# Kernel optimization log

Hardware: AMD Instinct MI355X
Metric: run time of the kernel (lower is better)

## Reference

```python
import jax, jax.numpy as jnp
import numpy as np

N = 100000   # nodes
E = 3200000  # edges
R = 8        # relations
F_IN = 128
DIMS = 64
C = 40


def setup_inputs() -> dict:
    key = jax.random.key(0)
    ks = jax.random.split(key, 10)
    s = 0.1
    return {
        "x": jax.random.normal(ks[0], (N, F_IN), jnp.float32),
        "edge_index": jax.random.randint(ks[1], (2, E), 0, N),
        "edge_weight": jax.random.uniform(ks[2], (E,), jnp.float32),
        "edge_color": jax.random.randint(ks[3], (E,), 0, R),
        "W1_rel": jax.random.normal(ks[4], (R, F_IN, DIMS), jnp.float32) * s,
        "W1_root": jax.random.normal(ks[5], (F_IN, DIMS), jnp.float32) * s,
        "b1": jnp.zeros((DIMS,), jnp.float32),
        "W2_rel": jax.random.normal(ks[6], (R, DIMS, C), jnp.float32) * s,
        "W2_root": jax.random.normal(ks[7], (DIMS, C), jnp.float32) * s,
        "b2": jnp.zeros((C,), jnp.float32),
    }


def _wrgcn_layer(x, src, dst, edge_weight, edge_color, W_rel, W_root, b):
    # Transform all nodes under every relation weight: [R, N, O]
    h = jnp.einsum('nf,rfo->rno', x, W_rel)
    # Gather per-edge message using (relation, source) indexing, weight it: [E, O]
    msg = h[edge_color, src] * edge_weight[:, None]
    # Scatter-add weighted messages to destination nodes
    agg = jnp.zeros((x.shape[0], W_rel.shape[2]), x.dtype).at[dst].add(msg)
    # Root (self) transform + bias
    return agg + x @ W_root + b


def reference(x, edge_index, edge_weight, edge_color, W1_rel, W1_root, b1, W2_rel, W2_root, b2):
    src, dst = edge_index[0], edge_index[1]
    h = jax.nn.relu(_wrgcn_layer(x, src, dst, edge_weight, edge_color, W1_rel, W1_root, b1))
    # dropout p=0 (eval): identity
    out = _wrgcn_layer(h, src, dst, edge_weight, edge_color, W2_rel, W2_root, b2)
    return (jax.nn.log_softmax(out, axis=1), out)
```

## Files before the change

kernel.cpp:

```cpp
#include <hip/hip_runtime.h>
#include <hip/hip_bf16.h>
#include <cmath>


#define RELS 8
#define CH 4096
#define ST2CAP 6144

typedef __attribute__((ext_vector_type(8))) short bf16x8;
typedef __attribute__((ext_vector_type(4))) float f32x4;

static __device__ __forceinline__ ushort f2bf(float f) {
    __hip_bfloat16 b = __float2bfloat16(f);
    return *reinterpret_cast<ushort*>(&b);
}
static __device__ __forceinline__ float bf2f(ushort u) {
    return __uint_as_float(((unsigned int)u) << 16);
}

__global__ __launch_bounds__(256) void cast_f32_bf16x4(
    const float* __restrict__ in, ushort* __restrict__ out, int n4)
{
    int i = blockIdx.x * 256 + threadIdx.x;
    if (i >= n4) return;
    float4 v = ((const float4*)in)[i];
    ushort4 o;
    o.x = f2bf(v.x); o.y = f2bf(v.y); o.z = f2bf(v.z); o.w = f2bf(v.w);
    ((ushort4*)out)[i] = o;
}

__global__ __launch_bounds__(256) void cast_relu_bf16x4(
    const float* __restrict__ in, ushort* __restrict__ out, int n4)
{
    int i = blockIdx.x * 256 + threadIdx.x;
    if (i >= n4) return;
    float4 v = ((const float4*)in)[i];
    ushort4 o;
    o.x = f2bf(fmaxf(v.x, 0.f)); o.y = f2bf(fmaxf(v.y, 0.f));
    o.z = f2bf(fmaxf(v.z, 0.f)); o.w = f2bf(fmaxf(v.w, 0.f));
    ((ushort4*)out)[i] = o;
}

__global__ __launch_bounds__(256) void conv_w1(
    const float* __restrict__ Wrel, const float* __restrict__ Wroot,
    ushort* __restrict__ wt)
{
    int i = blockIdx.x * 256 + threadIdx.x;
    if (i >= 9 * 64 * 128) return;
    int r = i >> 13, c = (i >> 7) & 63, k = i & 127;
    float v = (r < 8) ? Wrel[((size_t)r * 128 + k) * 64 + c]
                      : Wroot[(size_t)k * 64 + c];
    wt[i] = f2bf(v);
}

__global__ __launch_bounds__(256) void conv_w2(
    const float* __restrict__ Wrel, const float* __restrict__ Wroot,
    ushort* __restrict__ wt)
{
    int i = blockIdx.x * 256 + threadIdx.x;
    if (i >= 9 * 48 * 64) return;
    int r = i / (48 * 64), rem = i - r * (48 * 64);
    int c = rem >> 6, k = rem & 63;
    float v = 0.f;
    if (c < 40)
        v = (r < 8) ? Wrel[((size_t)r * 64 + k) * 40 + c]
                    : Wroot[(size_t)k * 40 + c];
    wt[i] = f2bf(v);
}

__global__ __launch_bounds__(256) void gemm1_mfma(
    const ushort* __restrict__ xb, const ushort* __restrict__ w1t,
    ushort* __restrict__ hout, float* __restrict__ agg1,
    const float* __restrict__ b1, int nN)
{
    __shared__ ushort xs[64 * 128];
    __shared__ ushort wt[64 * 128];
    const int y    = blockIdx.y;
    const int tid  = threadIdx.x;
    const int n0   = blockIdx.x * 64;
    const int nmax = nN - n0;
    const bool isroot = (y == 8);
    ushort* out = hout + (size_t)y * nN * 64;
    const ushort* wsrc = w1t + (size_t)y * 64 * 128;

    for (int i = tid; i < 1024; i += 256) {
        int row = i >> 4, ch = i & 15;
        uint4 v = make_uint4(0u, 0u, 0u, 0u);
        if (row < nmax)
            v = *(const uint4*)(xb + (size_t)(n0 + row) * 128 + ch * 8);
        int off = (row * 256 + ch * 16) ^ ((row & 7) << 4);
        *(uint4*)((char*)xs + off) = v;
    }
    for (int i = tid; i < 1024; i += 256) {
        int row = i >> 4, ch = i & 15;
        uint4 v = *(const uint4*)(wsrc + (size_t)row * 128 + ch * 8);
        int off = (row * 256 + ch * 16) ^ ((row & 7) << 4);
        *(uint4*)((char*)wt + off) = v;
    }
    __syncthreads();

    const int wv   = tid >> 6;
    const int lane = tid & 63;
    const int lr   = wv * 16 + (lane & 15);
    const int kgb  = (lane >> 4) * 8;

    f32x4 acc[4] = {{0.f,0.f,0.f,0.f},{0.f,0.f,0.f,0.f},
                    {0.f,0.f,0.f,0.f},{0.f,0.f,0.f,0.f}};

    #pragma unroll
    for (int ks = 0; ks < 4; ++ks) {
        int kb = (ks * 32 + kgb) * 2;
        int aoff = (lr * 256 + kb) ^ ((lr & 7) << 4);
        bf16x8 a = *(const bf16x8*)((const char*)xs + aoff);
        #pragma unroll
        for (int ct = 0; ct < 4; ++ct) {
            int col = ct * 16 + (lane & 15);
            int boff = (col * 256 + kb) ^ ((col & 7) << 4);
            bf16x8 b = *(const bf16x8*)((const char*)wt + boff);
            acc[ct] = __builtin_amdgcn_mfma_f32_16x16x32_bf16(a, b, acc[ct], 0, 0, 0);
        }
    }

    #pragma unroll
    for (int ct = 0; ct < 4; ++ct) {
        int col = ct * 16 + (lane & 15);
        #pragma unroll
        for (int reg = 0; reg < 4; ++reg) {
            int row = wv * 16 + (lane >> 4) * 4 + reg;
            if (row < nmax) {
                if (isroot)
                    agg1[(size_t)(n0 + row) * 64 + col] = acc[ct][reg] + b1[col];
                else
                    out[(size_t)(n0 + row) * 64 + col] = f2bf(acc[ct][reg]);
            }
        }
    }
}

__global__ __launch_bounds__(256) void gemm2_mfma(
    const ushort* __restrict__ y1b, const ushort* __restrict__ w2t,
    ushort* __restrict__ hout, float* __restrict__ agg2,
    const float* __restrict__ b2, int nN)
{
    __shared__ ushort ys[64 * 64];
    __shared__ ushort wt[48 * 64];
    const int y    = blockIdx.y;
    const int tid  = threadIdx.x;
    const int n0   = blockIdx.x * 64;
    const int nmax = nN - n0;
    const bool isroot = (y == 8);
    ushort* out = hout + (size_t)y * nN * 40;
    const ushort* wsrc = w2t + (size_t)y * 48 * 64;

    for (int i = tid; i < 512; i += 256) {
        int row = i >> 3, ch = i & 7;
        uint4 v = make_uint4(0u, 0u, 0u, 0u);
        if (row < nmax)
            v = *(const uint4*)(y1b + (size_t)(n0 + row) * 64 + ch * 8);
        int off = (row * 128 + ch * 16) ^ ((row & 7) << 4);
        *(uint4*)((char*)ys + off) = v;
    }
    for (int i = tid; i < 384; i += 256) {
        int row = i >> 3, ch = i & 7;
        uint4 v = *(const uint4*)(wsrc + (size_t)row * 64 + ch * 8);
        int off = (row * 128 + ch * 16) ^ ((row & 7) << 4);
        *(uint4*)((char*)wt + off) = v;
    }
    __syncthreads();

    const int wv   = tid >> 6;
    const int lane = tid & 63;
    const int lr   = wv * 16 + (lane & 15);
    const int kgb  = (lane >> 4) * 8;

    f32x4 acc[3] = {{0.f,0.f,0.f,0.f},{0.f,0.f,0.f,0.f},{0.f,0.f,0.f,0.f}};

    #pragma unroll
    for (int ks = 0; ks < 2; ++ks) {
        int kb = (ks * 32 + kgb) * 2;
        int aoff = (lr * 128 + kb) ^ ((lr & 7) << 4);
        bf16x8 a = *(const bf16x8*)((const char*)ys + aoff);
        #pragma unroll
        for (int ct = 0; ct < 3; ++ct) {
            int col = ct * 16 + (lane & 15);
            int boff = (col * 128 + kb) ^ ((col & 7) << 4);
            bf16x8 b = *(const bf16x8*)((const char*)wt + boff);
            acc[ct] = __builtin_amdgcn_mfma_f32_16x16x32_bf16(a, b, acc[ct], 0, 0, 0);
        }
    }

    #pragma unroll
    for (int ct = 0; ct < 3; ++ct) {
        int col = ct * 16 + (lane & 15);
        if (col < 40) {
            #pragma unroll
            for (int reg = 0; reg < 4; ++reg) {
                int row = wv * 16 + (lane >> 4) * 4 + reg;
                if (row < nmax) {
                    if (isroot)
                        agg2[(size_t)(n0 + row) * 40 + col] = acc[ct][reg] + b2[col];
                    else
                        out[(size_t)(n0 + row) * 40 + col] = f2bf(acc[ct][reg]);
                }
            }
        }
    }
}

__global__ __launch_bounds__(256) void mcount(
    const int* __restrict__ dst, int* __restrict__ cnt, int nE, int nBkt)
{
    __shared__ int hist[512];
    const int blk = blockIdx.x;
    const int t = threadIdx.x;
    for (int i = t; i < nBkt; i += 256) hist[i] = 0;
    __syncthreads();
    const int e0 = blk * CH;
    const int eend = min(e0 + CH, nE);
    for (int e = e0 + t; e < eend; e += 256)
        atomicAdd(&hist[dst[e] >> 8], 1);
    __syncthreads();
    for (int i = t; i < nBkt; i += 256)
        cnt[(size_t)blk * nBkt + i] = hist[i];
}

__global__ __launch_bounds__(1024) void scanB(
    const int* __restrict__ cnt, int* __restrict__ offm_rel,
    int* __restrict__ tsum, int nBlk, int nBkt)
{
    __shared__ int s[1024];
    const int bkt = blockIdx.x;
    const int t = threadIdx.x;
    int v = (t < nBlk) ? cnt[(size_t)t * nBkt + bkt] : 0;
    s[t] = v; __syncthreads();
    for (int o = 1; o < 1024; o <<= 1) {
        int u = (t >= o) ? s[t - o] : 0;
        __syncthreads(); s[t] += u; __syncthreads();
    }
    if (t < nBlk) offm_rel[(size_t)bkt * nBlk + t] = s[t] - v;
    if (t == nBlk - 1) tsum[bkt] = s[t];
}

__global__ __launch_bounds__(512) void scanT(
    const int* __restrict__ tsum, int* __restrict__ bktbase,
    int* __restrict__ row_off, int nBkt, int nN)
{
    __shared__ int s[512];
    const int t = threadIdx.x;
    int v = (t < nBkt) ? tsum[t] : 0;
    s[t] = v; __syncthreads();
    for (int o = 1; o < 512; o <<= 1) {
        int u = (t >= o) ? s[t - o] : 0;
        __syncthreads(); s[t] += u; __syncthreads();
    }
    if (t < nBkt) bktbase[t] = s[t] - v;
    if (t == nBkt - 1) { bktbase[nBkt] = s[t]; row_off[nN] = s[t]; }
}

__global__ __launch_bounds__(512) void mscatter(
    const int* __restrict__ src, const int* __restrict__ dst,
    const float* __restrict__ ew, const int* __restrict__ ec,
    const int* __restrict__ cnt, const int* __restrict__ offm_rel,
    const int* __restrict__ bktbase,
    uint2* __restrict__ epackA, int nE, int nBlk, int nBkt)
{
    __shared__ uint2 stag[CH];
    __shared__ int lbase[512];
    __shared__ int lcur[512];
    __shared__ int goff[512];
    const int blk = blockIdx.x;
    const int t = threadIdx.x;

    int v = (t < nBkt) ? cnt[(size_t)blk * nBkt + t] : 0;
    lbase[t] = v; __syncthreads();
    for (int o = 1; o < 512; o <<= 1) {
        int u = (t >= o) ? lbase[t - o] : 0;
        __syncthreads(); lbase[t] += u; __syncthreads();
    }
    int excl = lbase[t] - v;
    __syncthreads();
    lbase[t] = excl;
    lcur[t] = excl;
    goff[t] = (t < nBkt) ? bktbase[t] + offm_rel[(size_t)t * nBlk + blk] : 0;
    __syncthreads();

    const int e0 = blk * CH;
    const int eend = min(e0 + CH, nE);
    const int ntot = eend - e0;
    for (int e = e0 + t; e < eend; e += 512) {
        int d = dst[e];
        int bkt = d >> 8;
        unsigned int pk = (unsigned int)src[e] | ((unsigned int)ec[e] << 20)
                        | ((unsigned int)(d & 255) << 23);
        int r = atomicAdd(&lcur[bkt], 1);
        stag[r] = make_uint2(pk, __float_as_uint(ew[e]));
    }
    __syncthreads();
    for (int s2 = t; s2 < ntot; s2 += 512) {
        int lo = 0, hi = nBkt - 1;
        while (lo < hi) {
            int mid = (lo + hi + 1) >> 1;
            if (lbase[mid] <= s2) lo = mid; else hi = mid - 1;
        }
        epackA[goff[lo] + (s2 - lbase[lo])] = stag[s2];
    }
}

__global__ __launch_bounds__(256) void reorder2(
    const uint2* __restrict__ epackA, const int* __restrict__ bktbase,
    int* __restrict__ row_off, uint2* __restrict__ epack, int nN)
{
    __shared__ uint2 stag[ST2CAP];
    __shared__ int hist[256];
    __shared__ int s[256];
    __shared__ int lcur[128];
    const int b    = blockIdx.x;
    const int n0   = b << 7;
    const int pb   = b >> 1;
    const int half = b & 1;
    const int p0 = bktbase[pb];
    const int p1 = bktbase[pb + 1];
    const int t = threadIdx.x;

    hist[t] = 0;
    __syncthreads();
    const unsigned int* ax = (const unsigned int*)epackA;
    for (int e = p0 + t; e < p1; e += 256)
        atomicAdd(&hist[(ax[2 * (size_t)e] >> 23) & 255], 1);
    __syncthreads();
    int v = hist[t];
    s[t] = v; __syncthreads();
    for (int o = 1; o < 256; o <<= 1) {
        int u = (t >= o) ? s[t - o] : 0;
        __syncthreads(); s[t] += u; __syncthreads();
    }
    hist[t] = s[t] - v;
    __syncthreads();

    const int hb0 = hist[half << 7];
    const int hb1 = (half == 0) ? hist[128] : (p1 - p0);
    const int ne  = hb1 - hb0;
    const int s0  = p0 + hb0;

    if (t < 128) {
        int idx = n0 + t;
        if (idx < nN) row_off[idx] = p0 + hist[(half << 7) + t];
        lcur[t] = hist[(half << 7) + t] - hb0;
    }
    __syncthreads();

    if (ne <= ST2CAP) {
        for (int e = p0 + t; e < p1; e += 256) {
            uint2 pw = epackA[e];
            int dl = (pw.x >> 23) & 255;
            if ((dl >> 7) == half) {
                int r = atomicAdd(&lcur[dl & 127], 1);
                stag[r] = pw;
            }
        }
        __syncthreads();
        for (int s2 = t; s2 < ne; s2 += 256)
            epack[s0 + s2] = stag[s2];
    } else {
        if (t < 128) {
            int my = (half << 7) | t;
            int wpos = p0 + hist[my];
            for (int e = p0; e < p1; ++e) {
                uint2 pw = epackA[e];
                if ((int)((pw.x >> 23) & 255) == my) epack[wpos++] = pw;
            }
        }
    }
}

__global__ __launch_bounds__(256) void hist_dst(
    const int* __restrict__ dst, int* __restrict__ counts, int nE)
{
    int e = blockIdx.x * 256 + threadIdx.x;
    if (e < nE) atomicAdd(&counts[dst[e]], 1);
}

__global__ __launch_bounds__(256) void scan_partial(
    const int* __restrict__ counts, int* __restrict__ bsum, int nN)
{
    __shared__ int s[256];
    int t = threadIdx.x;
    int i = blockIdx.x * 256 + t;
    int v = (i < nN) ? counts[i] : 0;
    s[t] = v; __syncthreads();
    for (int o = 1; o < 256; o <<= 1) {
        int u = (t >= o) ? s[t - o] : 0;
        __syncthreads(); s[t] += u; __syncthreads();
    }
    if (t == 255) bsum[blockIdx.x] = s[255];
}

__global__ __launch_bounds__(512) void scan_base(
    const int* __restrict__ bsum, int* __restrict__ bbase, int nb,
    int* __restrict__ row_off, int nN)
{
    __shared__ int s[512];
    int t = threadIdx.x;
    int v = (t < nb) ? bsum[t] : 0;
    s[t] = v; __syncthreads();
    for (int o = 1; o < 512; o <<= 1) {
        int u = (t >= o) ? s[t - o] : 0;
        __syncthreads(); s[t] += u; __syncthreads();
    }
    if (t < nb) bbase[t] = s[t] - v;
    if (t == nb - 1) row_off[nN] = s[t];
}

__global__ __launch_bounds__(256) void scan_final(
    const int* __restrict__ counts, const int* __restrict__ bbase,
    int* __restrict__ row_off, int* __restrict__ cursor, int nN)
{
    __shared__ int s[256];
    int t = threadIdx.x;
    int i = blockIdx.x * 256 + t;
    int v = (i < nN) ? counts[i] : 0;
    s[t] = v; __syncthreads();
    for (int o = 1; o < 256; o <<= 1) {
        int u = (t >= o) ? s[t - o] : 0;
        __syncthreads(); s[t] += u; __syncthreads();
    }
    if (i < nN) {
        int off = bbase[blockIdx.x] + s[t] - v;
        row_off[i] = off;
        cursor[i]  = off;
    }
}

__global__ __launch_bounds__(256) void fill_csr(
    const int* __restrict__ src, const int* __restrict__ dst,
    const float* __restrict__ ew, const int* __restrict__ ec,
    int* __restrict__ cursor, uint2* __restrict__ epack, int nE)
{
    int e = blockIdx.x * 256 + threadIdx.x;
    if (e >= nE) return;
    int p = atomicAdd(&cursor[dst[e]], 1);
    epack[p] = make_uint2((unsigned int)src[e] | ((unsigned int)ec[e] << 20),
                          __float_as_uint(ew[e]));
}

__global__ __launch_bounds__(256) void gather_d64(
    const ushort* __restrict__ h, const int* __restrict__ row_off,
    const uint2* __restrict__ epack, float* __restrict__ agg, int nN)
{
    int w    = (blockIdx.x * 256 + threadIdx.x) >> 6;
    int lane = threadIdx.x & 63;
    if (w >= nN) return;
    int s0 = row_off[w], s1 = row_off[w + 1];
    float acc = agg[(size_t)w * 64 + lane];
    const unsigned int un = (unsigned int)nN;
    for (int base = s0; base < s1; base += 64) {
        int m = min(64, s1 - base);
        unsigned int pk = 0; float wv = 0.f;
        if (lane < m) {
            uint2 pw = epack[base + lane];
            pk = pw.x; wv = __uint_as_float(pw.y);
        }
        int j = 0;
        for (; j + 8 <= m; j += 8) {
            unsigned int p0 = __shfl(pk, j + 0, 64), p1 = __shfl(pk, j + 1, 64);
            unsigned int p2 = __shfl(pk, j + 2, 64), p3 = __shfl(pk, j + 3, 64);
            unsigned int p4 = __shfl(pk, j + 4, 64), p5 = __shfl(pk, j + 5, 64);
            unsigned int p6 = __shfl(pk, j + 6, 64), p7 = __shfl(pk, j + 7, 64);
            float q0 = __shfl(wv, j + 0, 64), q1 = __shfl(wv, j + 1, 64);
            float q2 = __shfl(wv, j + 2, 64), q3 = __shfl(wv, j + 3, 64);
            float q4 = __shfl(wv, j + 4, 64), q5 = __shfl(wv, j + 5, 64);
            float q6 = __shfl(wv, j + 6, 64), q7 = __shfl(wv, j + 7, 64);
            ushort v0 = h[(((p0 >> 20) & 7) * un + (p0 & 0xFFFFFu)) * 64u + lane];
            ushort v1 = h[(((p1 >> 20) & 7) * un + (p1 & 0xFFFFFu)) * 64u + lane];
            ushort v2 = h[(((p2 >> 20) & 7) * un + (p2 & 0xFFFFFu)) * 64u + lane];
            ushort v3 = h[(((p3 >> 20) & 7) * un + (p3 & 0xFFFFFu)) * 64u + lane];
            ushort v4 = h[(((p4 >> 20) & 7) * un + (p4 & 0xFFFFFu)) * 64u + lane];
            ushort v5 = h[(((p5 >> 20) & 7) * un + (p5 & 0xFFFFFu)) * 64u + lane];
            ushort v6 = h[(((p6 >> 20) & 7) * un + (p6 & 0xFFFFFu)) * 64u + lane];
            ushort v7 = h[(((p7 >> 20) & 7) * un + (p7 & 0xFFFFFu)) * 64u + lane];
            acc = fmaf(q0, bf2f(v0), acc); acc = fmaf(q1, bf2f(v1), acc);
            acc = fmaf(q2, bf2f(v2), acc); acc = fmaf(q3, bf2f(v3), acc);
            acc = fmaf(q4, bf2f(v4), acc); acc = fmaf(q5, bf2f(v5), acc);
            acc = fmaf(q6, bf2f(v6), acc); acc = fmaf(q7, bf2f(v7), acc);
        }
        for (; j < m; ++j) {
            unsigned int pj = __shfl(pk, j, 64);
            float        wj = __shfl(wv, j, 64);
            ushort v = h[(((pj >> 20) & 7) * un + (pj & 0xFFFFFu)) * 64u + lane];
            acc = fmaf(wj, bf2f(v), acc);
        }
    }
    agg[(size_t)w * 64 + lane] = acc;
}

__global__ __launch_bounds__(256) void gather_d40(
    const ushort* __restrict__ h, const int* __restrict__ row_off,
    const uint2* __restrict__ epack, float* __restrict__ agg, int nN)
{
    int w    = (blockIdx.x * 256 + threadIdx.x) >> 6;
    int lane = threadIdx.x & 63;
    if (w >= nN) return;
    int s0 = row_off[w], s1 = row_off[w + 1];
    float acc = 0.f;
    if (lane < 40) acc = agg[(size_t)w * 40 + lane];
    const unsigned int un = (unsigned int)nN;
    for (int base = s0; base < s1; base += 64) {
        int m = min(64, s1 - base);
        unsigned int pk = 0; float wv = 0.f;
        if (lane < m) {
            uint2 pw = epack[base + lane];
            pk = pw.x; wv = __uint_as_float(pw.y);
        }
        int j = 0;
        for (; j + 8 <= m; j += 8) {
            unsigned int p0 = __shfl(pk, j + 0, 64), p1 = __shfl(pk, j + 1, 64);
            unsigned int p2 = __shfl(pk, j + 2, 64), p3 = __shfl(pk, j + 3, 64);
            unsigned int p4 = __shfl(pk, j + 4, 64), p5 = __shfl(pk, j + 5, 64);
            unsigned int p6 = __shfl(pk, j + 6, 64), p7 = __shfl(pk, j + 7, 64);
            float q0 = __shfl(wv, j + 0, 64), q1 = __shfl(wv, j + 1, 64);
            float q2 = __shfl(wv, j + 2, 64), q3 = __shfl(wv, j + 3, 64);
            float q4 = __shfl(wv, j + 4, 64), q5 = __shfl(wv, j + 5, 64);
            float q6 = __shfl(wv, j + 6, 64), q7 = __shfl(wv, j + 7, 64);
            if (lane < 40) {
                ushort v0 = h[(((p0 >> 20) & 7) * un + (p0 & 0xFFFFFu)) * 40u + lane];
                ushort v1 = h[(((p1 >> 20) & 7) * un + (p1 & 0xFFFFFu)) * 40u + lane];
                ushort v2 = h[(((p2 >> 20) & 7) * un + (p2 & 0xFFFFFu)) * 40u + lane];
                ushort v3 = h[(((p3 >> 20) & 7) * un + (p3 & 0xFFFFFu)) * 40u + lane];
                ushort v4 = h[(((p4 >> 20) & 7) * un + (p4 & 0xFFFFFu)) * 40u + lane];
                ushort v5 = h[(((p5 >> 20) & 7) * un + (p5 & 0xFFFFFu)) * 40u + lane];
                ushort v6 = h[(((p6 >> 20) & 7) * un + (p6 & 0xFFFFFu)) * 40u + lane];
                ushort v7 = h[(((p7 >> 20) & 7) * un + (p7 & 0xFFFFFu)) * 40u + lane];
                acc = fmaf(q0, bf2f(v0), acc); acc = fmaf(q1, bf2f(v1), acc);
                acc = fmaf(q2, bf2f(v2), acc); acc = fmaf(q3, bf2f(v3), acc);
                acc = fmaf(q4, bf2f(v4), acc); acc = fmaf(q5, bf2f(v5), acc);
                acc = fmaf(q6, bf2f(v6), acc); acc = fmaf(q7, bf2f(v7), acc);
            }
        }
        for (; j < m; ++j) {
            unsigned int pj = __shfl(pk, j, 64);
            float        wj = __shfl(wv, j, 64);
            if (lane < 40) {
                ushort v = h[(((pj >> 20) & 7) * un + (pj & 0xFFFFFu)) * 40u + lane];
                acc = fmaf(wj, bf2f(v), acc);
            }
        }
    }
    if (lane < 40) agg[(size_t)w * 40 + lane] = acc;
}

__global__ __launch_bounds__(256) void logsoftmax_out(
    const float* __restrict__ agg2, float* __restrict__ out, int nN)
{
    int w    = (blockIdx.x * 256 + threadIdx.x) >> 6;
    int lane = threadIdx.x & 63;
    if (w >= nN) return;
    float v = -INFINITY;
    if (lane < 40) v = agg2[(size_t)w * 40 + lane];
    float m = v;
    #pragma unroll
    for (int o = 32; o > 0; o >>= 1) m = fmaxf(m, __shfl_xor(m, o, 64));
    float ex = (lane < 40) ? expf(v - m) : 0.f;
    float s = ex;
    #pragma unroll
    for (int o = 32; o > 0; o >>= 1) s += __shfl_xor(s, o, 64);
    float lse = logf(s) + m;
    if (lane < 40) {
        out[(size_t)w * 40 + lane] = v - lse;
        out[(size_t)nN * 40 + (size_t)w * 40 + lane] = v;
    }
}

extern "C" void kernel_launch(void* const* d_in, const int* in_sizes, int n_in,
                              void* d_out, int out_size, void* d_ws, size_t ws_size,
                              hipStream_t stream)
{
    const float* x       = (const float*)d_in[0];
    const int*   eidx    = (const int*)  d_in[1];
    const float* ew      = (const float*)d_in[2];
    const int*   ec      = (const int*)  d_in[3];
    const float* W1_rel  = (const float*)d_in[4];
    const float* W1_root = (const float*)d_in[5];
    const float* b1      = (const float*)d_in[6];
    const float* W2_rel  = (const float*)d_in[7];
    const float* W2_root = (const float*)d_in[8];
    const float* b2      = (const float*)d_in[9];

    const int nN = in_sizes[0] / 128;
    const int nE = in_sizes[2];
    const int* src = eidx;
    const int* dst = eidx + nE;

    const int nBkt = (nN + 255) >> 8;
    const int nBlk = (nE + CH - 1) / CH;

    char* w8 = (char*)d_ws;
    size_t off = 0;
    auto alloc = [&](size_t bytes) {
        void* p = w8 + off;
        off += (bytes + 255) & ~(size_t)255;
        return p;
    };
    ushort* h      = (ushort*)alloc((size_t)RELS * nN * 64 * 2);
    ushort* xb     = (ushort*)alloc((size_t)nN * 128 * 2);
    float*  agg1   = (float*) alloc((size_t)nN * 64 * 4);
    float*  agg2   = (float*) alloc((size_t)nN * 40 * 4);
    int*    counts = (int*)   alloc((size_t)nN * 4);
    int*    row_off= (int*)   alloc(((size_t)nN + 1) * 4);
    int*    cursor = (int*)   alloc((size_t)nN * 4);
    int*    tsum   = (int*)   alloc(4096);
    int*    bktbase= (int*)   alloc(4096);
    uint2*  epack  = (uint2*) alloc((size_t)nE * 8);
    ushort* w1t    = (ushort*)alloc((size_t)9 * 64 * 128 * 2);
    ushort* w2t    = (ushort*)alloc((size_t)9 * 48 * 64 * 2);
    int*    cnt    = (int*)   alloc((size_t)nBlk * nBkt * 4);
    int*    offm   = (int*)   alloc((size_t)nBkt * nBlk * 4);
    uint2*  epackA = (uint2*) alloc((size_t)nE * 8);
    const bool multisplit = (off <= ws_size) && (nBlk <= 1024) && (nBkt <= 512)
                            && (nN < (1 << 20));
    ushort* y1b = xb;

    const dim3 blk(256);
    const int NB_scan     = (nN + 255) / 256;
    const int gemm_blocks = (nN + 63) / 64;
    const int edge_blocks = (nE + 255) / 256;
    const int wave_blocks = (int)(((size_t)nN * 64 + 255) / 256);
    const int ls_blocks   = (nN + 3) / 4;

    if (multisplit) {
        mcount<<<nBlk, blk, 0, stream>>>(dst, cnt, nE, nBkt);
        scanB<<<nBkt, dim3(1024), 0, stream>>>(cnt, offm, tsum, nBlk, nBkt);
        scanT<<<1, dim3(512), 0, stream>>>(tsum, bktbase, row_off, nBkt, nN);
        mscatter<<<nBlk, dim3(512), 0, stream>>>(src, dst, ew, ec, cnt, offm,
                                                 bktbase, epackA, nE, nBlk, nBkt);
        reorder2<<<(nN + 127) / 128, blk, 0, stream>>>(epackA, bktbase,
                                                       row_off, epack, nN);
    } else {
        hipMemsetAsync(counts, 0, (size_t)nN * 4, stream);
        hist_dst<<<edge_blocks, blk, 0, stream>>>(dst, counts, nE);
        scan_partial<<<NB_scan, blk, 0, stream>>>(counts, tsum, nN);
        scan_base<<<1, dim3(512), 0, stream>>>(tsum, bktbase, NB_scan, row_off, nN);
        scan_final<<<NB_scan, blk, 0, stream>>>(counts, bktbase, row_off, cursor, nN);
        fill_csr<<<edge_blocks, blk, 0, stream>>>(src, dst, ew, ec, cursor, epack, nE);
    }

    cast_f32_bf16x4<<<(nN * 128 / 4 + 255) / 256, blk, 0, stream>>>(x, xb, nN * 128 / 4);
    conv_w1<<<(9 * 64 * 128 + 255) / 256, blk, 0, stream>>>(W1_rel, W1_root, w1t);
    conv_w2<<<(9 * 48 * 64 + 255) / 256, blk, 0, stream>>>(W2_rel, W2_root, w2t);

    gemm1_mfma<<<dim3(gemm_blocks, 9), blk, 0, stream>>>(xb, w1t, h, agg1, b1, nN);
    gather_d64<<<wave_blocks, blk, 0, stream>>>(h, row_off, epack, agg1, nN);

    cast_relu_bf16x4<<<(nN * 64 / 4 + 255) / 256, blk, 0, stream>>>(agg1, y1b, nN * 64 / 4);
    gemm2_mfma<<<dim3(gemm_blocks, 9), blk, 0, stream>>>(y1b, w2t, h, agg2, b2, nN);
    gather_d40<<<wave_blocks, blk, 0, stream>>>(h, row_off, epack, agg2, nN);

    logsoftmax_out<<<ls_blocks, blk, 0, stream>>>(agg2, (float*)d_out, nN);
}
```

Baseline: 419.7 us.

## Fuse relu-cast and log-softmax into gathers; process multiple edges per wave

The first-layer gather now applies ReLU and writes bf16 directly, which removes the separate cast kernel and the fp32 agg1 write-back. The second-layer gather computes log-softmax in-register and writes both outputs, which drops the logsoftmax kernel. Both gathers now load two bf16 values per lane with 32-bit loads and split the wave into sub-groups that each handle a different edge (2 groups for d64, 3 groups of 20 for d40). A cross-group shuffle reduction combines the partial sums. This aims to cut memory traffic and idle lanes, at the cost of extra shuffles and more complex tail handling.

```diff
diff --git a/kernel.cpp b/kernel.cpp
--- a/kernel.cpp
+++ b/kernel.cpp
@@ -13,9 +13,6 @@
 static __device__ __forceinline__ ushort f2bf(float f) {
     __hip_bfloat16 b = __float2bfloat16(f);
     return *reinterpret_cast<ushort*>(&b);
-}
-static __device__ __forceinline__ float bf2f(ushort u) {
-    return __uint_as_float(((unsigned int)u) << 16);
 }
 
 __global__ __launch_bounds__(256) void cast_f32_bf16x4(
@@ -26,18 +23,6 @@
     float4 v = ((const float4*)in)[i];
     ushort4 o;
     o.x = f2bf(v.x); o.y = f2bf(v.y); o.z = f2bf(v.z); o.w = f2bf(v.w);
-    ((ushort4*)out)[i] = o;
-}
-
-__global__ __launch_bounds__(256) void cast_relu_bf16x4(
-    const float* __restrict__ in, ushort* __restrict__ out, int n4)
-{
-    int i = blockIdx.x * 256 + threadIdx.x;
-    if (i >= n4) return;
-    float4 v = ((const float4*)in)[i];
-    ushort4 o;
-    o.x = f2bf(fmaxf(v.x, 0.f)); o.y = f2bf(fmaxf(v.y, 0.f));
-    o.z = f2bf(fmaxf(v.z, 0.f)); o.w = f2bf(fmaxf(v.w, 0.f));
     ((ushort4*)out)[i] = o;
 }
 
@@ -443,16 +428,25 @@
                           __float_as_uint(ew[e]));
 }
 
-__global__ __launch_bounds__(256) void gather_d64(
+__global__ __launch_bounds__(256) void gather_relu_d64(
     const ushort* __restrict__ h, const int* __restrict__ row_off,
-    const uint2* __restrict__ epack, float* __restrict__ agg, int nN)
+    const uint2* __restrict__ epack, const float* __restrict__ agg1,
+    ushort* __restrict__ y1b, int nN)
 {
     int w    = (blockIdx.x * 256 + threadIdx.x) >> 6;
     int lane = threadIdx.x & 63;
     if (w >= nN) return;
+    const int half = lane >> 5;
+    const int hl   = lane & 31;
+    const unsigned int un = (unsigned int)nN;
     int s0 = row_off[w], s1 = row_off[w + 1];
-    float acc = agg[(size_t)w * 64 + lane];
-    const unsigned int un = (unsigned int)nN;
+
+    float a0 = 0.f, a1 = 0.f;
+    if (half == 0) {
+        float2 iv = *(const float2*)(agg1 + (size_t)w * 64 + 2 * hl);
+        a0 = iv.x; a1 = iv.y;
+    }
+
     for (int base = s0; base < s1; base += 64) {
         int m = min(64, s1 - base);
         unsigned int pk = 0; float wv = 0.f;
@@ -462,48 +456,72 @@
         }
         int j = 0;
         for (; j + 8 <= m; j += 8) {
-            unsigned int p0 = __shfl(pk, j + 0, 64), p1 = __shfl(pk, j + 1, 64);
-            unsigned int p2 = __shfl(pk, j + 2, 64), p3 = __shfl(pk, j + 3, 64);
-            unsigned int p4 = __shfl(pk, j + 4, 64), p5 = __shfl(pk, j + 5, 64);
-            unsigned int p6 = __shfl(pk, j + 6, 64), p7 = __shfl(pk, j + 7, 64);
-            float q0 = __shfl(wv, j + 0, 64), q1 = __shfl(wv, j + 1, 64);
-            float q2 = __shfl(wv, j + 2, 64), q3 = __shfl(wv, j + 3, 64);
-            float q4 = __shfl(wv, j + 4, 64), q5 = __shfl(wv, j + 5, 64);
-            float q6 = __shfl(wv, j + 6, 64), q7 = __shfl(wv, j + 7, 64);
-            ushort v0 = h[(((p0 >> 20) & 7) * un + (p0 & 0xFFFFFu)) * 64u + lane];
-            ushort v1 = h[(((p1 >> 20) & 7) * un + (p1 & 0xFFFFFu)) * 64u + lane];
-            ushort v2 = h[(((p2 >> 20) & 7) * un + (p2 & 0xFFFFFu)) * 64u + lane];
-            ushort v3 = h[(((p3 >> 20) & 7) * un + (p3 & 0xFFFFFu)) * 64u + lane];
-            ushort v4 = h[(((p4 >> 20) & 7) * un + (p4 & 0xFFFFFu)) * 64u + lane];
-            ushort v5 = h[(((p5 >> 20) & 7) * un + (p5 & 0xFFFFFu)) * 64u + lane];
-            ushort v6 = h[(((p6 >> 20) & 7) * un + (p6 & 0xFFFFFu)) * 64u + lane];
-            ushort v7 = h[(((p7 >> 20) & 7) * un + (p7 & 0xFFFFFu)) * 64u + lane];
-            acc = fmaf(q0, bf2f(v0), acc); acc = fmaf(q1, bf2f(v1), acc);
-            acc = fmaf(q2, bf2f(v2), acc); acc = fmaf(q3, bf2f(v3), acc);
-            acc = fmaf(q4, bf2f(v4), acc); acc = fmaf(q5, bf2f(v5), acc);
-            acc = fmaf(q6, bf2f(v6), acc); acc = fmaf(q7, bf2f(v7), acc);
-        }
-        for (; j < m; ++j) {
-            unsigned int pj = __shfl(pk, j, 64);
-            float        wj = __shfl(wv, j, 64);
-            ushort v = h[(((pj >> 20) & 7) * un + (pj & 0xFFFFFu)) * 64u + lane];
-            acc = fmaf(wj, bf2f(v), acc);
-        }
-    }
-    agg[(size_t)w * 64 + lane] = acc;
-}
-
-__global__ __launch_bounds__(256) void gather_d40(
+            unsigned int pA = __shfl(pk, j + 0 + half, 64);
+            unsigned int pB = __shfl(pk, j + 2 + half, 64);
+            unsigned int pC = __shfl(pk, j + 4 + half, 64);
+            unsigned int pD = __shfl(pk, j + 6 + half, 64);
+            float qA = __shfl(wv, j + 0 + half, 64);
+            float qB = __shfl(wv, j + 2 + half, 64);
+            float qC = __shfl(wv, j + 4 + half, 64);
+            float qD = __shfl(wv, j + 6 + half, 64);
+            unsigned int vA = *(const unsigned int*)(h + ((((pA >> 20) & 7) * un + (pA & 0xFFFFFu)) * 64u + 2u * hl));
+            unsigned int vB = *(const unsigned int*)(h + ((((pB >> 20) & 7) * un + (pB & 0xFFFFFu)) * 64u + 2u * hl));
+            unsigned int vC = *(const unsigned int*)(h + ((((pC >> 20) & 7) * un + (pC & 0xFFFFFu)) * 64u + 2u * hl));
+            unsigned int vD = *(const unsigned int*)(h + ((((pD >> 20) & 7) * un + (pD & 0xFFFFFu)) * 64u + 2u * hl));
+            a0 = fmaf(qA, __uint_as_float(vA << 16), a0);
+            a1 = fmaf(qA, __uint_as_float(vA & 0xFFFF0000u), a1);
+            a0 = fmaf(qB, __uint_as_float(vB << 16), a0);
+            a1 = fmaf(qB, __uint_as_float(vB & 0xFFFF0000u), a1);
+            a0 = fmaf(qC, __uint_as_float(vC << 16), a0);
+            a1 = fmaf(qC, __uint_as_float(vC & 0xFFFF0000u), a1);
+            a0 = fmaf(qD, __uint_as_float(vD << 16), a0);
+            a1 = fmaf(qD, __uint_as_float(vD & 0xFFFF0000u), a1);
+        }
+        for (; j + 2 <= m; j += 2) {
+            unsigned int p = __shfl(pk, j + half, 64);
+            float q = __shfl(wv, j + half, 64);
+            unsigned int v = *(const unsigned int*)(h + ((((p >> 20) & 7) * un + (p & 0xFFFFFu)) * 64u + 2u * hl));
+            a0 = fmaf(q, __uint_as_float(v << 16), a0);
+            a1 = fmaf(q, __uint_as_float(v & 0xFFFF0000u), a1);
+        }
+        if (j < m) {
+            unsigned int p = __shfl(pk, j, 64);
+            float q = __shfl(wv, j, 64);
+            if (half == 0) {
+                unsigned int v = *(const unsigned int*)(h + ((((p >> 20) & 7) * un + (p & 0xFFFFFu)) * 64u + 2u * hl));
+                a0 = fmaf(q, __uint_as_float(v << 16), a0);
+                a1 = fmaf(q, __uint_as_float(v & 0xFFFF0000u), a1);
+            }
+        }
+    }
+    a0 += __shfl_xor(a0, 32, 64);
+    a1 += __shfl_xor(a1, 32, 64);
+    if (half == 0) {
+        unsigned int b0 = f2bf(fmaxf(a0, 0.f));
+        unsigned int b1 = f2bf(fmaxf(a1, 0.f));
+        *(unsigned int*)(y1b + (size_t)w * 64 + 2 * hl) = b0 | (b1 << 16);
+    }
+}
+
+__global__ __launch_bounds__(256) void gather_lsm_d40(
     const ushort* __restrict__ h, const int* __restrict__ row_off,
-    const uint2* __restrict__ epack, float* __restrict__ agg, int nN)
+    const uint2* __restrict__ epack, const float* __restrict__ agg2,
+    float* __restrict__ out, int nN)
 {
     int w    = (blockIdx.x * 256 + threadIdx.x) >> 6;
     int lane = threadIdx.x & 63;
     if (w >= nN) return;
+    const int g  = lane / 20;
+    const int hl = lane - g * 20;
+    const unsigned int un = (unsigned int)nN;
     int s0 = row_off[w], s1 = row_off[w + 1];
-    float acc = 0.f;
-    if (lane < 40) acc = agg[(size_t)w * 40 + lane];
-    const unsigned int un = (unsigned int)nN;
+
+    float a0 = 0.f, a1 = 0.f;
+    if (g == 0) {
+        float2 iv = *(const float2*)(agg2 + (size_t)w * 40 + 2 * hl);
+        a0 = iv.x; a1 = iv.y;
+    }
+
     for (int base = s0; base < s1; base += 64) {
         int m = min(64, s1 - base);
         unsigned int pk = 0; float wv = 0.f;
@@ -512,61 +530,51 @@
             pk = pw.x; wv = __uint_as_float(pw.y);
         }
         int j = 0;
-        for (; j + 8 <= m; j += 8) {
-            unsigned int p0 = __shfl(pk, j + 0, 64), p1 = __shfl(pk, j + 1, 64);
-            unsigned int p2 = __shfl(pk, j + 2, 64), p3 = __shfl(pk, j + 3, 64);
-            unsigned int p4 = __shfl(pk, j + 4, 64), p5 = __shfl(pk, j + 5, 64);
-            unsigned int p6 = __shfl(pk, j + 6, 64), p7 = __shfl(pk, j + 7, 64);
-            float q0 = __shfl(wv, j + 0, 64), q1 = __shfl(wv, j + 1, 64);
-            float q2 = __shfl(wv, j + 2, 64), q3 = __shfl(wv, j + 3, 64);
-            float q4 = __shfl(wv, j + 4, 64), q5 = __shfl(wv, j + 5, 64);
-            float q6 = __shfl(wv, j + 6, 64), q7 = __shfl(wv, j + 7, 64);
-            if (lane < 40) {
-                ushort v0 = h[(((p0 >> 20) & 7) * un + (p0 & 0xFFFFFu)) * 40u + lane];
-                ushort v1 = h[(((p1 >> 20) & 7) * un + (p1 & 0xFFFFFu)) * 40u + lane];
-                ushort v2 = h[(((p2 >> 20) & 7) * un + (p2 & 0xFFFFFu)) * 40u + lane];
-                ushort v3 = h[(((p3 >> 20) & 7) * un + (p3 & 0xFFFFFu)) * 40u + lane];
-                ushort v4 = h[(((p4 >> 20) & 7) * un + (p4 & 0xFFFFFu)) * 40u + lane];
-                ushort v5 = h[(((p5 >> 20) & 7) * un + (p5 & 0xFFFFFu)) * 40u + lane];
-                ushort v6 = h[(((p6 >> 20) & 7) * un + (p6 & 0xFFFFFu)) * 40u + lane];
-                ushort v7 = h[(((p7 >> 20) & 7) * un + (p7 & 0xFFFFFu)) * 40u + lane];
-                acc = fmaf(q0, bf2f(v0), acc); acc = fmaf(q1, bf2f(v1), acc);
-                acc = fmaf(q2, bf2f(v2), acc); acc = fmaf(q3, bf2f(v3), acc);
-                acc = fmaf(q4, bf2f(v4), acc); acc = fmaf(q5, bf2f(v5), acc);
-                acc = fmaf(q6, bf2f(v6), acc); acc = fmaf(q7, bf2f(v7), acc);
+        for (; j + 6 <= m; j += 6) {
+            unsigned int pA = __shfl(pk, j + g, 64);
+            unsigned int pB = __shfl(pk, j + 3 + g, 64);
+            float qA = __shfl(wv, j + g, 64);
+            float qB = __shfl(wv, j + 3 + g, 64);
+            unsigned int vA = *(const unsigned int*)(h + ((((pA >> 20) & 7) * un + (pA & 0xFFFFFu)) * 40u + 2u * hl));
+            unsigned int vB = *(const unsigned int*)(h + ((((pB >> 20) & 7) * un + (pB & 0xFFFFFu)) * 40u + 2u * hl));
+            a0 = fmaf(qA, __uint_as_float(vA << 16), a0);
+            a1 = fmaf(qA, __uint_as_float(vA & 0xFFFF0000u), a1);
+            a0 = fmaf(qB, __uint_as_float(vB << 16), a0);
+            a1 = fmaf(qB, __uint_as_float(vB & 0xFFFF0000u), a1);
+        }
+        for (; j + 3 <= m; j += 3) {
+            unsigned int p = __shfl(pk, j + g, 64);
+            float q = __shfl(wv, j + g, 64);
+            unsigned int v = *(const unsigned int*)(h + ((((p >> 20) & 7) * un + (p & 0xFFFFFu)) * 40u + 2u * hl));
+            a0 = fmaf(q, __uint_as_float(v << 16), a0);
+            a1 = fmaf(q, __uint_as_float(v & 0xFFFF0000u), a1);
+        }
+        for (; j < m; ++j) {
+            unsigned int p = __shfl(pk, j, 64);
+            float q = __shfl(wv, j, 64);
+            if (g == 0) {
+                unsigned int v = *(const unsigned int*)(h + ((((p >> 20) & 7) * un + (p & 0xFFFFFu)) * 40u + 2u * hl));
+                a0 = fmaf(q, __uint_as_float(v << 16), a0);
+                a1 = fmaf(q, __uint_as_float(v & 0xFFFF0000u), a1);
             }
         }
-        for (; j < m; ++j) {
-            unsigned int pj = __shfl(pk, j, 64);
-            float        wj = __shfl(wv, j, 64);
-            if (lane < 40) {
-                ushort v = h[(((pj >> 20) & 7) * un + (pj & 0xFFFFFu)) * 40u + lane];
-                acc = fmaf(wj, bf2f(v), acc);
-            }
-        }
-    }
-    if (lane < 40) agg[(size_t)w * 40 + lane] = acc;
-}
-
-__global__ __launch_bounds__(256) void logsoftmax_out(
-    const float* __restrict__ agg2, float* __restrict__ out, int nN)
-{
-    int w    = (blockIdx.x * 256 + threadIdx.x) >> 6;
-    int lane = threadIdx.x & 63;
-    if (w >= nN) return;
-    float v = -INFINITY;
-    if (lane < 40) v = agg2[(size_t)w * 40 + lane];
-    float m = v;
+    }
+    float b0 = __shfl(a0, hl + 20, 64), c0 = __shfl(a0, hl + 40, 64);
+    float b1 = __shfl(a1, hl + 20, 64), c1 = __shfl(a1, hl + 40, 64);
+    a0 += b0 + c0;
+    a1 += b1 + c1;
+
+    float mx = (g == 0) ? fmaxf(a0, a1) : -INFINITY;
     #pragma unroll
-    for (int o = 32; o > 0; o >>= 1) m = fmaxf(m, __shfl_xor(m, o, 64));
-    float ex = (lane < 40) ? expf(v - m) : 0.f;
-    float s = ex;
+    for (int o = 32; o > 0; o >>= 1) mx = fmaxf(mx, __shfl_xor(mx, o, 64));
+    float ex = (g == 0) ? (expf(a0 - mx) + expf(a1 - mx)) : 0.f;
     #pragma unroll
-    for (int o = 32; o > 0; o >>= 1) s += __shfl_xor(s, o, 64);
-    float lse = logf(s) + m;
-    if (lane < 40) {
-        out[(size_t)w * 40 + lane] = v - lse;
-        out[(size_t)nN * 40 + (size_t)w * 40 + lane] = v;
+    for (int o = 32; o > 0; o >>= 1) ex += __shfl_xor(ex, o, 64);
+    float lse = logf(ex) + mx;
+
+    if (g == 0) {
+        *(float2*)(out + (size_t)w * 40 + 2 * hl) = make_float2(a0 - lse, a1 - lse);
+        *(float2*)(out + (size_t)nN * 40 + (size_t)w * 40 + 2 * hl) = make_float2(a0, a1);
     }
 }
 
@@ -624,7 +632,6 @@
     const int gemm_blocks = (nN + 63) / 64;
     const int edge_blocks = (nE + 255) / 256;
     const int wave_blocks = (int)(((size_t)nN * 64 + 255) / 256);
-    const int ls_blocks   = (nN + 3) / 4;
 
     if (multisplit) {
         mcount<<<nBlk, blk, 0, stream>>>(dst, cnt, nE, nBkt);
@@ -648,11 +655,9 @@
     conv_w2<<<(9 * 48 * 64 + 255) / 256, blk, 0, stream>>>(W2_rel, W2_root, w2t);
 
     gemm1_mfma<<<dim3(gemm_blocks, 9), blk, 0, stream>>>(xb, w1t, h, agg1, b1, nN);
-    gather_d64<<<wave_blocks, blk, 0, stream>>>(h, row_off, epack, agg1, nN);
-
-    cast_relu_bf16x4<<<(nN * 64 / 4 + 255) / 256, blk, 0, stream>>>(agg1, y1b, nN * 64 / 4);
+    gather_relu_d64<<<wave_blocks, blk, 0, stream>>>(h, row_off, epack, agg1, y1b, nN);
+
     gemm2_mfma<<<dim3(gemm_blocks, 9), blk, 0, stream>>>(y1b, w2t, h, agg2, b2, nN);
-    gather_d40<<<wave_blocks, blk, 0, stream>>>(h, row_off, epack, agg2, nN);
-
-    logsoftmax_out<<<ls_blocks, blk, 0, stream>>>(agg2, (float*)d_out, nN);
-}
+    gather_lsm_d40<<<wave_blocks, blk, 0, stream>>>(h, row_off, epack, agg2,
+                                                    (float*)d_out, nN);
+}
```

After: 386.8 us. 7.8% less time.
